# Performance work log

Measured on AMD Instinct MI355X. Metric: run time of the kernel, lower is better.

## Reference

```python
import jax, jax.numpy as jnp
import numpy as np
from jax import lax

B, L, V = 128, 64, 8192
E = H = 128
STEPS = 10
MAX_BIN = 512
BETA_START, BETA_END = 1e-4, 2e-2


def setup_inputs():
    key = jax.random.key(0)
    k = jax.random.split(key, 23)
    s = 0.05
    padded_x = (jax.random.uniform(k[0], (B, L, V)) < 0.01).astype(jnp.float32)
    lengths = jax.random.randint(k[1], (B,), 1, L + 1)
    visit_mask = (jnp.arange(L)[None, :] < lengths[:, None]).astype(jnp.float32)
    padded_bins = jnp.sort(jax.random.randint(k[2], (B, L), 0, MAX_BIN), axis=1)
    t_diff = jax.random.randint(k[3], (B,), 1, STEPS + 1)
    eps = jax.random.normal(k[4], (B, L, E))
    z0 = jax.random.normal(k[5], (B, L, E))
    noise = jax.random.normal(k[6], (STEPS, B, L, E))
    W_visit = jax.random.normal(k[7], (E, V)) * s
    bin_embed = (jax.random.normal(k[8], (MAX_BIN + 2, E)) * s).at[0].set(0.0)  # padding_idx=0
    W_ih = jax.random.normal(k[9], (4 * H, E)) * s
    W_hh = jax.random.normal(k[10], (4 * H, H)) * s
    b_ih = jax.random.normal(k[11], (4 * H,)) * s
    b_hh = jax.random.normal(k[12], (4 * H,)) * s
    W_cls = jax.random.normal(k[13], (1, H)) * s
    b_cls = jax.random.normal(k[14], (1,)) * s
    W_proj = jax.random.normal(k[15], (E, H)) * s
    time_embed = jax.random.normal(k[16], (STEPS + 1, E)) * s
    W_fuse = jax.random.normal(k[17], (2, 2 * E)) * s
    b_fuse = jax.random.normal(k[18], (2,)) * s
    W_e1 = jax.random.normal(k[19], (E, 2 * E)) * s
    b_e1 = jax.random.normal(k[20], (E,)) * s
    W_e2 = jax.random.normal(k[21], (E, E)) * s
    b_e2 = jax.random.normal(k[22], (E,)) * s
    return dict(padded_x=padded_x, visit_mask=visit_mask, padded_bins=padded_bins,
                t_diff=t_diff, eps=eps, z0=z0, noise=noise, W_visit=W_visit,
                bin_embed=bin_embed, W_ih=W_ih, W_hh=W_hh, b_ih=b_ih, b_hh=b_hh,
                W_cls=W_cls, b_cls=b_cls, W_proj=W_proj, time_embed=time_embed,
                W_fuse=W_fuse, b_fuse=b_fuse, W_e1=W_e1, b_e1=b_e1, W_e2=W_e2, b_e2=b_e2)


def _lstm(v, W_ih, W_hh, b_ih, b_hh):
    # v: [B,L,E] -> h: [B,L,H]; PyTorch gate order i,f,g,o
    xg = jnp.einsum('ble,ge->blg', v, W_ih) + b_ih + b_hh
    def step(carry, x):
        h, c = carry
        g = x + h @ W_hh.T
        i, f, gg, o = jnp.split(g, 4, axis=-1)
        c = jax.nn.sigmoid(f) * c + jax.nn.sigmoid(i) * jnp.tanh(gg)
        h = jax.nn.sigmoid(o) * jnp.tanh(c)
        return (h, c), h
    z = jnp.zeros((v.shape[0], W_hh.shape[1]), v.dtype)
    _, hs = lax.scan(step, (z, z), jnp.swapaxes(xg, 0, 1))
    return jnp.swapaxes(hs, 0, 1)


def _last_hidden(h, mask):
    lengths = jnp.maximum(mask.sum(axis=1).astype(jnp.int32), 1)
    return h[jnp.arange(h.shape[0]), lengths - 1]


def reference(padded_x, visit_mask, padded_bins, t_diff, eps, z0, noise,
              W_visit, bin_embed, W_ih, W_hh, b_ih, b_hh, W_cls, b_cls,
              W_proj, time_embed, W_fuse, b_fuse, W_e1, b_e1, W_e2, b_e2):
    m = visit_mask[..., None]                      # [B,L,1]
    betas = jnp.linspace(BETA_START, BETA_END, STEPS)
    alphas = 1.0 - betas
    alpha_bars = jnp.cumprod(alphas)

    # visit embedding + time-gap (delta bin) embedding
    delta = jnp.concatenate([jnp.zeros_like(padded_bins[:, :1]),
                             jnp.clip(padded_bins[:, 1:] - padded_bins[:, :-1], 0)], axis=1)
    delta = jnp.where(visit_mask > 0, jnp.clip(delta, 0, MAX_BIN + 1), 0)
    v = (padded_x @ W_visit.T + bin_embed[delta]) * m  # [B,L,E]

    # encoder LSTM (packed seq == plain scan then zero padded suffix positions)
    h = _lstm(v, W_ih, W_hh, b_ih, b_hh) * m
    logits_real = (_last_hidden(h, visit_mask) @ W_cls.T + b_cls)[:, 0]

    h_prev = jnp.pad(h[:, :-1], ((0, 0), (1, 0), (0, 0)))
    hp = (h_prev @ W_proj.T) * m                   # [B,L,E]

    def fuse_eps(z, t_emb):
        a = jax.nn.softmax(jnp.concatenate([z, hp], -1) @ W_fuse.T + b_fuse, axis=-1)
        g = a[..., :1] * z + a[..., 1:] * hp
        x = jnp.concatenate([g, t_emb], -1)
        return jax.nn.relu(x @ W_e1.T + b_e1) @ W_e2.T + b_e2

    # diffusion loss
    t = jnp.where(visit_mask > 0, t_diff[:, None], 1)    # [B,L]
    ab = alpha_bars[t - 1][..., None]
    z_t = (jnp.sqrt(ab) * v + jnp.sqrt(1.0 - ab) * eps) * m
    eps_pred = fuse_eps(z_t, time_embed[t])
    denom = jnp.maximum(visit_mask.sum(), 1.0)
    diffusion_loss = jnp.sum((eps_pred - eps) ** 2 * m) / denom

    # reverse diffusion sampling of synthetic visit embeddings
    def step(z, inp):
        kk, nz = inp
        t_s = jnp.where(visit_mask > 0, kk, 1)
        e = fuse_eps(z, time_embed[t_s])
        beta = betas[kk - 1]
        mean = (z - beta / jnp.sqrt(1.0 - alpha_bars[kk - 1]) * e) / jnp.sqrt(alphas[kk - 1])
        z = jnp.where(kk > 1, mean + jnp.sqrt(beta) * nz, mean) * m
        return z, None

    ks = jnp.arange(STEPS, 0, -1)
    v_syn, _ = lax.scan(step, z0, (ks, noise))

    h_syn = _lstm(v_syn, W_ih, W_hh, b_ih, b_hh) * m
    logits_syn = (_last_hidden(h_syn, visit_mask) @ W_cls.T + b_cls)[:, 0]
    return logits_real, logits_syn, diffusion_loss
```

## Files before the change

### kernel.cpp

```cpp
#include <hip/hip_runtime.h>

#define B_ 128
#define L_ 64
#define V_ 8192
#define E_ 128
#define H_ 128
#define G4_ 512
#define NROW (B_*L_)
#define HSTRIDE 136
#define AS 136
#define XS 264
#define YS 136
#define ZS 132

typedef unsigned short u16;
typedef __attribute__((ext_vector_type(8))) short bf16x8;
typedef __attribute__((ext_vector_type(4))) float f32x4;

__device__ __forceinline__ float sigm(float x){ return 1.f/(1.f + __expf(-x)); }
__device__ __forceinline__ float ftanh(float x){ float e = __expf(2.f*x); return 1.f - 2.f/(e + 1.f); }
__device__ __forceinline__ u16 f2bf(float f){
    union { unsigned int i; float f; } x; x.f = f;
    unsigned int r = x.i + 0x7fff + ((x.i >> 16) & 1);
    return (u16)(r >> 16);
}
#define LBAR() asm volatile("s_waitcnt lgkmcnt(0)\ns_barrier" ::: "memory")

__device__ __forceinline__ bf16x8 pack8(const float* p){
    const float4* q = (const float4*)p;
    float4 a = q[0], b = q[1];
    bf16x8 f;
    f[0]=(short)f2bf(a.x); f[1]=(short)f2bf(a.y); f[2]=(short)f2bf(a.z); f[3]=(short)f2bf(a.w);
    f[4]=(short)f2bf(b.x); f[5]=(short)f2bf(b.y); f[6]=(short)f2bf(b.z); f[7]=(short)f2bf(b.w);
    return f;
}

__global__ __launch_bounds__(256) void k_transpose_wv(const float* __restrict__ Wv, float* __restrict__ WT){
    __shared__ float tile[16][129];
    int v0 = blockIdx.x * 16;
    int t = threadIdx.x;
    #pragma unroll
    for(int i=0;i<8;i++){
        int idx = i*256 + t; int e = idx >> 4; int vv = idx & 15;
        tile[vv][e] = Wv[(size_t)e*V_ + v0 + vv];
    }
    __syncthreads();
    #pragma unroll
    for(int i=0;i<8;i++){
        int idx = i*256 + t; int vv = idx >> 7; int e = idx & 127;
        WT[(size_t)(v0+vv)*E_ + e] = tile[vv][e];
    }
}

__global__ __launch_bounds__(256) void k_visit_embed(const float* __restrict__ px, const float* __restrict__ vmask,
                                                     const int* __restrict__ bins, const float* __restrict__ bemb,
                                                     const float* __restrict__ WT, float* __restrict__ v){
    __shared__ int idxs[512];
    __shared__ int cnt;
    __shared__ int dsh;
    __shared__ float msh;
    __shared__ float4 red[8][32];
    int row = blockIdx.x; int l = row & 63;
    int t = threadIdx.x;
    if(t==0){
        cnt = 0;
        float m = vmask[row];
        int d = 0;
        if(l > 0){ d = bins[row] - bins[row-1]; d = d < 0 ? 0 : (d > 513 ? 513 : d); }
        if(!(m > 0.f)) d = 0;
        dsh = d; msh = m;
    }
    __syncthreads();
    const uint4* xr4 = (const uint4*)(px + (size_t)row * V_);
    for(int i=t;i<2048;i+=256){
        uint4 u = xr4[i];
        unsigned int w[4] = {u.x,u.y,u.z,u.w};
        #pragma unroll
        for(int j=0;j<4;j++){
            if(w[j]){ int p = atomicAdd(&cnt,1); if(p<512) idxs[p] = i*4 + j; }
        }
    }
    __syncthreads();
    int n = cnt; if(n > 512) n = 512;
    int eq = t & 31, jg = t >> 5;
    float4 a4 = {0.f,0.f,0.f,0.f};
    for(int j=jg;j<n;j+=8){
        const float4* wr = (const float4*)(WT + (size_t)idxs[j]*E_);
        float4 wv = wr[eq];
        a4.x += wv.x; a4.y += wv.y; a4.z += wv.z; a4.w += wv.w;
    }
    red[jg][eq] = a4;
    __syncthreads();
    if(t < 32){
        float4 s = red[0][t];
        #pragma unroll
        for(int g=1;g<8;g++){
            float4 r = red[g][t];
            s.x += r.x; s.y += r.y; s.z += r.z; s.w += r.w;
        }
        const float4* bp = (const float4*)(bemb + dsh*E_);
        float4 bv = bp[t];
        float m = msh;
        float4 o;
        o.x = (s.x + bv.x)*m; o.y = (s.y + bv.y)*m; o.z = (s.z + bv.z)*m; o.w = (s.w + bv.w)*m;
        ((float4*)(v + (size_t)row*E_))[t] = o;
    }
}

__global__ __launch_bounds__(256,2) void k_gemm_xg(const float* __restrict__ A, const float* __restrict__ Wih,
                                                   const float* __restrict__ bih, const float* __restrict__ bhh,
                                                   float* __restrict__ xg){
    __shared__ __align__(16) u16 abuf[16*AS];
    int t = threadIdx.x, wave = t >> 6, lane = t & 63, quad = lane >> 4, lc = lane & 15;
    int row0 = blockIdx.x * 16;
    #pragma unroll
    for(int i=0;i<8;i++){
        int flat = i*256 + t; int r = flat >> 7, e = flat & 127;
        abuf[r*AS + e] = f2bf(A[(size_t)(row0+r)*E_ + e]);
    }
    bf16x8 wfr[8][4]; float bb[8];
    #pragma unroll
    for(int nt=0;nt<8;nt++){
        int n = wave*128 + nt*16 + lc;
        bb[nt] = bih[n] + bhh[n];
        const float* wr = Wih + (size_t)n*E_ + quad*8;
        #pragma unroll
        for(int kt=0;kt<4;kt++) wfr[nt][kt] = pack8(wr + kt*32);
    }
    __syncthreads();
    f32x4 acc[8];
    #pragma unroll
    for(int nt=0;nt<8;nt++) acc[nt] = (f32x4){0.f,0.f,0.f,0.f};
    #pragma unroll
    for(int kt=0;kt<4;kt++){
        bf16x8 af = *(const bf16x8*)&abuf[lc*AS + kt*32 + quad*8];
        #pragma unroll
        for(int nt=0;nt<8;nt++)
            acc[nt] = __builtin_amdgcn_mfma_f32_16x16x32_bf16(af, wfr[nt][kt], acc[nt], 0,0,0);
    }
    #pragma unroll
    for(int nt=0;nt<8;nt++){
        int n = wave*128 + nt*16 + lc;
        #pragma unroll
        for(int r=0;r<4;r++)
            xg[(size_t)(row0 + quad*4 + r)*G4_ + n] = acc[nt][r] + bb[nt];
    }
}

__device__ __forceinline__ void lstm_step(int l, const float* pxg, float* hp_out, bool dohp,
        const u16* bufr, u16* bufw, const bf16x8 (&bf)[4][4], const bf16x8 (&wp)[4],
        float (&xcur)[4][4], float (&xnxt)[4][4], float (&c4)[4], float (&lg4)[4],
        const int (&len4)[4], float wcv,
        const float* vmsh, int lc, int quad, int wave, int b0){
    if(l+1 < 64){
        #pragma unroll
        for(int gate=0;gate<4;gate++){
            #pragma unroll
            for(int r=0;r<4;r++)
                xnxt[gate][r] = pxg[(size_t)r*64*G4_ + (size_t)(l+1)*G4_ + gate*128];
        }
    }
    bf16x8 af[4];
    #pragma unroll
    for(int kt=0;kt<4;kt++)
        af[kt] = *(const bf16x8*)&bufr[lc*HSTRIDE + kt*32 + quad*8];
    f32x4 acc[4], acch;
    #pragma unroll
    for(int a=0;a<4;a++) acc[a] = (f32x4){0.f,0.f,0.f,0.f};
    acch = (f32x4){0.f,0.f,0.f,0.f};
    #pragma unroll
    for(int kt=0;kt<4;kt++){
        #pragma unroll
        for(int a=0;a<4;a++)
            acc[a] = __builtin_amdgcn_mfma_f32_16x16x32_bf16(af[kt], bf[a][kt], acc[a], 0,0,0);
        acch = __builtin_amdgcn_mfma_f32_16x16x32_bf16(af[kt], wp[kt], acch, 0,0,0);
    }
    if(dohp){
        #pragma unroll
        for(int r=0;r<4;r++){
            float m = vmsh[(quad*4+r)*64 + l];
            int grow = (b0 + quad*4 + r)*64 + l;
            hp_out[(size_t)grow*E_ + wave*16 + lc] = acch[r] * m;
        }
    }
    #pragma unroll
    for(int r=0;r<4;r++){
        float gi = acc[0][r] + xcur[0][r];
        float gf = acc[1][r] + xcur[1][r];
        float gg = acc[2][r] + xcur[2][r];
        float go = acc[3][r] + xcur[3][r];
        float c  = sigm(gf)*c4[r] + sigm(gi)*ftanh(gg);
        float h  = sigm(go)*ftanh(c);
        c4[r] = c;
        bufw[(quad*4+r)*HSTRIDE + wave*16 + lc] = f2bf(h);
        if(l == len4[r]-1) lg4[r] += h * wcv;
    }
    LBAR();
}

__global__ __launch_bounds__(512,2) void k_lstm_fused(const float* __restrict__ xg, const float* __restrict__ Whh,
        const float* __restrict__ Wproj, const float* __restrict__ Wcls, const float* __restrict__ bcls,
        const float* __restrict__ vmask, float* __restrict__ hp_out, float* __restrict__ logits_out){
    __shared__ u16 hbuf[2][16*HSTRIDE];
    __shared__ float vmsh[16*64];
    __shared__ int lensh[16];
    __shared__ float lgsh[16][132];
    int t = threadIdx.x;
    int wave = t >> 6, lane = t & 63;
    int quad = lane >> 4, lc = lane & 15;
    int b0 = blockIdx.x * 16;
    bool dohp = (hp_out != nullptr);

    for(int i=t;i<16*HSTRIDE;i+=512) hbuf[0][i] = 0;
    for(int i=t;i<1024;i+=512) vmsh[i] = vmask[b0*64 + i];
    __syncthreads();
    if(t < 16){
        int s = 0;
        #pragma unroll
        for(int i=0;i<64;i++) s += (vmsh[t*64 + i] > 0.f) ? 1 : 0;
        lensh[t] = s < 1 ? 1 : s;
    }

    int cw = wave*16 + lc;
    bf16x8 bf[4][4];
    #pragma unroll
    for(int gate=0;gate<4;gate++){
        int n = gate*128 + cw;
        const float* wr = Whh + (size_t)n*H_ + quad*8;
        #pragma unroll
        for(int kt=0;kt<4;kt++) bf[gate][kt] = pack8(wr + kt*32);
    }
    bf16x8 wp[4];
    {
        const float* wr = Wproj + (size_t)cw*H_ + quad*8;
        #pragma unroll
        for(int kt=0;kt<4;kt++) wp[kt] = pack8(wr + kt*32);
    }
    float wcv = Wcls[cw];

    float c4[4] = {0.f,0.f,0.f,0.f};
    float lg4[4] = {0.f,0.f,0.f,0.f};

    const float* pxg = xg + ((size_t)(b0 + quad*4))*64*G4_ + cw;

    float xgv0[4][4], xgv1[4][4];
    #pragma unroll
    for(int gate=0;gate<4;gate++){
        #pragma unroll
        for(int r=0;r<4;r++)
            xgv0[gate][r] = pxg[(size_t)r*64*G4_ + gate*128];
    }
    __syncthreads();
    int len4[4];
    #pragma unroll
    for(int r=0;r<4;r++) len4[r] = lensh[quad*4 + r];

    for(int lb=0;lb<64;lb+=2){
        lstm_step(lb,   pxg, hp_out, dohp, hbuf[0], hbuf[1], bf, wp, xgv0, xgv1, c4, lg4, len4, wcv, vmsh, lc, quad, wave, b0);
        lstm_step(lb+1, pxg, hp_out, dohp, hbuf[1], hbuf[0], bf, wp, xgv1, xgv0, c4, lg4, len4, wcv, vmsh, lc, quad, wave, b0);
    }
    #pragma unroll
    for(int r=0;r<4;r++) lgsh[quad*4+r][cw] = lg4[r];
    __syncthreads();
    {
        int row = t >> 5, l32 = t & 31;
        float s = lgsh[row][l32] + lgsh[row][l32+32] + lgsh[row][l32+64] + lgsh[row][l32+96];
        s += __shfl_down(s, 16, 32);
        s += __shfl_down(s, 8, 32);
        s += __shfl_down(s, 4, 32);
        s += __shfl_down(s, 2, 32);
        s += __shfl_down(s, 1, 32);
        if(l32 == 0) logits_out[b0 + row] = s + bcls[0];
    }
}

__global__ __launch_bounds__(256,2) void k_drg(const float* __restrict__ v, const float* __restrict__ hp,
        const float* __restrict__ eps, const int* __restrict__ tdiff, const float* __restrict__ vmask,
        const float* __restrict__ z0, const float* __restrict__ noise, const float* __restrict__ temb,
        const float* __restrict__ Wf, const float* __restrict__ bfu,
        const float* __restrict__ We1, const float* __restrict__ be1,
        const float* __restrict__ We2, const float* __restrict__ be2,
        const float* __restrict__ Wih, const float* __restrict__ bih, const float* __restrict__ bhh,
        float* __restrict__ partial, float* __restrict__ xg2){
    __shared__ float zbuf[16*ZS], hpbuf[16*ZS];
    __shared__ __align__(16) u16 xbuf[16*XS];
    __shared__ __align__(16) u16 y1buf[16*YS];
    __shared__ float wfsh[512];
    __shared__ float ssh[16][2], hpd[16][2];
    __shared__ float mrow[16]; __shared__ int trow[16];
    __shared__ float sbeta[10], sabar[10];
    __shared__ float rb[4];
    int row0 = blockIdx.x * 16; int t = threadIdx.x;
    int wave = t >> 6, lane = t & 63, quad = lane >> 4, lc = lane & 15;

    if(t==0){
        float p = 1.f;
        for(int k=0;k<10;k++){ float b = 1e-4f + (0.02f - 1e-4f)*k/9.f; sbeta[k] = b; p *= (1.f - b); sabar[k] = p; }
    }
    if(t < 16){
        int row = row0 + t; float m = vmask[row];
        mrow[t] = m; trow[t] = (m > 0.f) ? tdiff[row >> 6] : 1;
    }
    for(int i=t;i<512;i+=256) wfsh[i] = Wf[i];
    __syncthreads();
    #pragma unroll
    for(int i=0;i<8;i++){
        int flat = i*256 + t; int r = flat >> 7; int e = flat & 127; int row = row0 + r;
        float ab = sabar[trow[r]-1];
        zbuf[r*ZS + e] = (sqrtf(ab)*v[(size_t)row*E_ + e] + sqrtf(1.f - ab)*eps[(size_t)row*E_ + e]) * mrow[r];
        hpbuf[r*ZS + e] = hp[(size_t)row*E_ + e];
    }
    bf16x8 wf1[2][8], wf2[2][4];
    float be1v[2], be2v[2];
    #pragma unroll
    for(int nt=0;nt<2;nt++){
        int n = wave*32 + nt*16 + lc;
        be1v[nt] = be1[n]; be2v[nt] = be2[n];
        const float* w1 = We1 + (size_t)n*256 + quad*8;
        #pragma unroll
        for(int kt=0;kt<8;kt++) wf1[nt][kt] = pack8(w1 + kt*32);
        const float* w2 = We2 + (size_t)n*128 + quad*8;
        #pragma unroll
        for(int kt=0;kt<4;kt++) wf2[nt][kt] = pack8(w2 + kt*32);
    }
    __syncthreads();
    {
        int row = t >> 4, k = (t >> 3) & 1, sub = t & 7;
        float p = 0.f;
        #pragma unroll
        for(int i=0;i<16;i++)
            p += hpbuf[row*ZS + sub*16 + i] * wfsh[k*256 + 128 + sub*16 + i];
        p += __shfl_down(p,4); p += __shfl_down(p,2); p += __shfl_down(p,1);
        if(sub == 0) hpd[row][k] = p + bfu[k];
    }
    __syncthreads();

    for(int s=0;s<11;s++){
        int kk = 10 - (s - 1);
        {
            int row = t >> 4, k = (t >> 3) & 1, sub = t & 7;
            float q = 0.f;
            #pragma unroll
            for(int i=0;i<16;i++)
                q += zbuf[row*ZS + sub*16 + i] * wfsh[k*256 + sub*16 + i];
            q += __shfl_down(q,4); q += __shfl_down(q,2); q += __shfl_down(q,1);
            if(sub == 0) ssh[row][k] = q + hpd[row][k];
        }
        __syncthreads();
        {
            int row = t >> 4, c0 = (t & 15) * 16;
            float s0 = ssh[row][0], s1 = ssh[row][1];
            float a0 = 1.f/(1.f + __expf(s1 - s0)), a1 = 1.f - a0;
            int tt = (s == 0) ? trow[row] : ((mrow[row] > 0.f) ? kk : 1);
            #pragma unroll
            for(int i=0;i<16;i++){
                int c = c0 + i;
                float val = (c < 128) ? (a0*zbuf[row*ZS + c] + a1*hpbuf[row*ZS + c])
                                      : temb[tt*E_ + (c - 128)];
                xbuf[row*XS + c] = f2bf(val);
            }
        }
        __syncthreads();
        f32x4 acc1[2];
        acc1[0] = (f32x4){0.f,0.f,0.f,0.f}; acc1[1] = (f32x4){0.f,0.f,0.f,0.f};
        #pragma unroll
        for(int kt=0;kt<8;kt++){
            bf16x8 af = *(const bf16x8*)&xbuf[lc*XS + kt*32 + quad*8];
            acc1[0] = __builtin_amdgcn_mfma_f32_16x16x32_bf16(af, wf1[0][kt], acc1[0], 0,0,0);
            acc1[1] = __builtin_amdgcn_mfma_f32_16x16x32_bf16(af, wf1[1][kt], acc1[1], 0,0,0);
        }
        #pragma unroll
        for(int nt=0;nt<2;nt++){
            #pragma unroll
            for(int r=0;r<4;r++)
                y1buf[(quad*4+r)*YS + wave*32 + nt*16 + lc] = f2bf(fmaxf(acc1[nt][r] + be1v[nt], 0.f));
        }
        __syncthreads();
        f32x4 acc2[2];
        acc2[0] = (f32x4){0.f,0.f,0.f,0.f}; acc2[1] = (f32x4){0.f,0.f,0.f,0.f};
        #pragma unroll
        for(int kt=0;kt<4;kt++){
            bf16x8 af = *(const bf16x8*)&y1buf[lc*YS + kt*32 + quad*8];
            acc2[0] = __builtin_amdgcn_mfma_f32_16x16x32_bf16(af, wf2[0][kt], acc2[0], 0,0,0);
            acc2[1] = __builtin_amdgcn_mfma_f32_16x16x32_bf16(af, wf2[1][kt], acc2[1], 0,0,0);
        }
        if(s == 0){
            float lp = 0.f;
            #pragma unroll
            for(int nt=0;nt<2;nt++){
                int n = wave*32 + nt*16 + lc;
                #pragma unroll
                for(int r=0;r<4;r++){
                    int m = quad*4 + r;
                    float d = (acc2[nt][r] + be2v[nt]) - eps[(size_t)(row0+m)*E_ + n];
                    lp += d*d*mrow[m];
                }
            }
            #pragma unroll
            for(int off=32;off;off>>=1) lp += __shfl_down(lp, off);
            if(lane == 0) rb[wave] = lp;
            __syncthreads();
            if(t == 0) partial[blockIdx.x] = rb[0]+rb[1]+rb[2]+rb[3];
            #pragma unroll
            for(int i=0;i<8;i++){
                int flat = i*256 + t; int r = flat >> 7; int e = flat & 127;
                zbuf[r*ZS + e] = z0[(size_t)(row0+r)*E_ + e];
            }
            __syncthreads();
        } else {
            float beta = sbeta[kk-1];
            float c1 = beta / sqrtf(1.f - sabar[kk-1]);
            float c2 = 1.f / sqrtf(1.f - beta);
            float sb = sqrtf(beta);
            #pragma unroll
            for(int nt=0;nt<2;nt++){
                int n = wave*32 + nt*16 + lc;
                #pragma unroll
                for(int r=0;r<4;r++){
                    int m = quad*4 + r;
                    float e = acc2[nt][r] + be2v[nt];
                    float z = zbuf[m*ZS + n];
                    float mean = (z - c1*e) * c2;
                    float nz = noise[((size_t)(s-1)*NROW + row0 + m)*E_ + n];
                    float znew = (kk > 1) ? (mean + sb*nz) : mean;
                    zbuf[m*ZS + n] = znew * mrow[m];
                }
            }
            __syncthreads();
        }
    }
    {
        int row = t >> 4, c0 = (t & 15) * 8;
        #pragma unroll
        for(int i=0;i<8;i++)
            xbuf[row*XS + c0 + i] = f2bf(zbuf[row*ZS + c0 + i]);
    }
    __syncthreads();
    bf16x8 wg[8][4]; float bb[8];
    #pragma unroll
    for(int nt=0;nt<8;nt++){
        int n = wave*128 + nt*16 + lc;
        bb[nt] = bih[n] + bhh[n];
        const float* wr = Wih + (size_t)n*E_ + quad*8;
        #pragma unroll
        for(int kt=0;kt<4;kt++) wg[nt][kt] = pack8(wr + kt*32);
    }
    f32x4 ac[8];
    #pragma unroll
    for(int nt=0;nt<8;nt++) ac[nt] = (f32x4){0.f,0.f,0.f,0.f};
    #pragma unroll
    for(int kt=0;kt<4;kt++){
        bf16x8 af = *(const bf16x8*)&xbuf[lc*XS + kt*32 + quad*8];
        #pragma unroll
        for(int nt=0;nt<8;nt++)
            ac[nt] = __builtin_amdgcn_mfma_f32_16x16x32_bf16(af, wg[nt][kt], ac[nt], 0,0,0);
    }
    #pragma unroll
    for(int nt=0;nt<8;nt++){
        int n = wave*128 + nt*16 + lc;
        #pragma unroll
        for(int r=0;r<4;r++)
            xg2[(size_t)(row0 + quad*4 + r)*G4_ + n] = ac[nt][r] + bb[nt];
    }
}

__global__ void k_finalize(const float* __restrict__ partial, const float* __restrict__ vmask, float* __restrict__ out){
    __shared__ float rb[4], rl[4];
    int t = threadIdx.x;
    float s = 0.f;
    for(int i=t;i<NROW;i+=256) s += vmask[i];
    float ls = 0.f;
    for(int i=t;i<512;i+=256) ls += partial[i];
    #pragma unroll
    for(int off=32;off;off>>=1){ s += __shfl_down(s, off); ls += __shfl_down(ls, off); }
    if((t & 63) == 0){ rb[t >> 6] = s; rl[t >> 6] = ls; }
    __syncthreads();
    if(t == 0){
        float denom = rb[0]+rb[1]+rb[2]+rb[3];
        if(denom < 1.f) denom = 1.f;
        out[256] = (rl[0]+rl[1]+rl[2]+rl[3]) / denom;
    }
}

extern "C" void kernel_launch(void* const* d_in, const int* in_sizes, int n_in,
                              void* d_out, int out_size, void* d_ws, size_t ws_size,
                              hipStream_t stream){
    const float* px    = (const float*)d_in[0];
    const float* vmask = (const float*)d_in[1];
    const int*   bins  = (const int*)d_in[2];
    const int*   tdiff = (const int*)d_in[3];
    const float* eps   = (const float*)d_in[4];
    const float* z0    = (const float*)d_in[5];
    const float* noise = (const float*)d_in[6];
    const float* Wv    = (const float*)d_in[7];
    const float* bemb  = (const float*)d_in[8];
    const float* Wih   = (const float*)d_in[9];
    const float* Whh   = (const float*)d_in[10];
    const float* bih   = (const float*)d_in[11];
    const float* bhh   = (const float*)d_in[12];
    const float* Wcls  = (const float*)d_in[13];
    const float* bcls  = (const float*)d_in[14];
    const float* Wproj = (const float*)d_in[15];
    const float* temb  = (const float*)d_in[16];
    const float* Wf    = (const float*)d_in[17];
    const float* bfu   = (const float*)d_in[18];
    const float* We1   = (const float*)d_in[19];
    const float* be1   = (const float*)d_in[20];
    const float* We2   = (const float*)d_in[21];
    const float* be2   = (const float*)d_in[22];
    float* out = (float*)d_out;

    float* ws      = (float*)d_ws;
    float* WT      = ws;
    float* v       = ws + 1048576;
    float* xg      = ws + 2097152;
    float* hp      = ws + 6291456;
    float* partial = ws + 7340032;

    hipLaunchKernelGGL(k_transpose_wv, dim3(V_/16), dim3(256), 0, stream, Wv, WT);
    hipLaunchKernelGGL(k_visit_embed, dim3(NROW), dim3(256), 0, stream, px, vmask, bins, bemb, WT, v);
    hipLaunchKernelGGL(k_gemm_xg, dim3(NROW/16), dim3(256), 0, stream, v, Wih, bih, bhh, xg);
    hipLaunchKernelGGL(k_lstm_fused, dim3(B_/16), dim3(512), 0, stream,
                       xg, Whh, Wproj, Wcls, bcls, vmask, hp, out);
    hipLaunchKernelGGL(k_drg, dim3(NROW/16), dim3(256), 0, stream,
                       v, hp, eps, tdiff, vmask, z0, noise, temb, Wf, bfu,
                       We1, be1, We2, be2, Wih, bih, bhh, partial, xg);
    hipLaunchKernelGGL(k_lstm_fused, dim3(B_/16), dim3(512), 0, stream,
                       xg, Whh, Wproj, Wcls, bcls, vmask, (float*)nullptr, out + 128);
    hipLaunchKernelGGL(k_finalize, dim3(1), dim3(256), 0, stream, partial, vmask, out);
}
```

Baseline: 816.3 us.

## Fuse LSTM input projection into recurrent kernel and drop xg buffers

Removes the separate input-gate GEMM kernel and the tail GEMM in the diffusion kernel. The LSTM kernel now stages each timestep's visit embedding in shared memory as bf16 and computes W_ih·v alongside W_hh·h with MFMA inside the recurrence, so the large xg gate tensor no longer has to be written and re-read from global memory. The LSTM kernel is templated on whether the projected hidden state is needed, which drops the projection MFMAs in the second pass. The diffusion kernel loads its noise, eps and z0 values into registers at the start of each step and writes v_syn directly. The trade-off is that each serial LSTM step now carries twice the MFMA work on the critical recurrent path, with only 8 blocks running. The hp output also no longer multiplies by the visit mask.

Result: no change. 824.1 us (+1.0%).

```diff
diff --git a/kernel.cpp b/kernel.cpp
--- a/kernel.cpp
+++ b/kernel.cpp
@@ -5,7 +5,6 @@
 #define V_ 8192
 #define E_ 128
 #define H_ 128
-#define G4_ 512
 #define NROW (B_*L_)
 #define HSTRIDE 136
 #define AS 136
@@ -107,112 +106,86 @@
     }
 }
 
-__global__ __launch_bounds__(256,2) void k_gemm_xg(const float* __restrict__ A, const float* __restrict__ Wih,
-                                                   const float* __restrict__ bih, const float* __restrict__ bhh,
-                                                   float* __restrict__ xg){
-    __shared__ __align__(16) u16 abuf[16*AS];
-    int t = threadIdx.x, wave = t >> 6, lane = t & 63, quad = lane >> 4, lc = lane & 15;
-    int row0 = blockIdx.x * 16;
-    #pragma unroll
-    for(int i=0;i<8;i++){
-        int flat = i*256 + t; int r = flat >> 7, e = flat & 127;
-        abuf[r*AS + e] = f2bf(A[(size_t)(row0+r)*E_ + e]);
-    }
-    bf16x8 wfr[8][4]; float bb[8];
-    #pragma unroll
-    for(int nt=0;nt<8;nt++){
-        int n = wave*128 + nt*16 + lc;
-        bb[nt] = bih[n] + bhh[n];
-        const float* wr = Wih + (size_t)n*E_ + quad*8;
-        #pragma unroll
-        for(int kt=0;kt<4;kt++) wfr[nt][kt] = pack8(wr + kt*32);
-    }
-    __syncthreads();
-    f32x4 acc[8];
-    #pragma unroll
-    for(int nt=0;nt<8;nt++) acc[nt] = (f32x4){0.f,0.f,0.f,0.f};
+template<bool DOHP>
+__device__ __forceinline__ void lstm_step(int l,
+        const u16* __restrict__ bufr, u16* __restrict__ bufw,
+        const u16* __restrict__ vbr, u16* __restrict__ vbw,
+        const float*& pv, float*& hpb,
+        const bf16x8 (&bfh)[4][4], const bf16x8 (&bfv)[4][4], const bf16x8 (&wp)[4],
+        const float (&bb)[4], float (&c4)[4], float (&lg4)[4], const int (&len4)[4],
+        float wcv, int t, int lc, int quad, int cw){
+    float4 vnx;
+    if(l+1 < 64){ vnx = *(const float4*)pv; pv += E_; }
+    bf16x8 afh[4], afv[4];
     #pragma unroll
     for(int kt=0;kt<4;kt++){
-        bf16x8 af = *(const bf16x8*)&abuf[lc*AS + kt*32 + quad*8];
-        #pragma unroll
-        for(int nt=0;nt<8;nt++)
-            acc[nt] = __builtin_amdgcn_mfma_f32_16x16x32_bf16(af, wfr[nt][kt], acc[nt], 0,0,0);
-    }
-    #pragma unroll
-    for(int nt=0;nt<8;nt++){
-        int n = wave*128 + nt*16 + lc;
-        #pragma unroll
-        for(int r=0;r<4;r++)
-            xg[(size_t)(row0 + quad*4 + r)*G4_ + n] = acc[nt][r] + bb[nt];
-    }
-}
-
-__device__ __forceinline__ void lstm_step(int l, const float* pxg, float* hp_out, bool dohp,
-        const u16* bufr, u16* bufw, const bf16x8 (&bf)[4][4], const bf16x8 (&wp)[4],
-        float (&xcur)[4][4], float (&xnxt)[4][4], float (&c4)[4], float (&lg4)[4],
-        const int (&len4)[4], float wcv,
-        const float* vmsh, int lc, int quad, int wave, int b0){
-    if(l+1 < 64){
-        #pragma unroll
-        for(int gate=0;gate<4;gate++){
-            #pragma unroll
-            for(int r=0;r<4;r++)
-                xnxt[gate][r] = pxg[(size_t)r*64*G4_ + (size_t)(l+1)*G4_ + gate*128];
-        }
-    }
-    bf16x8 af[4];
-    #pragma unroll
-    for(int kt=0;kt<4;kt++)
-        af[kt] = *(const bf16x8*)&bufr[lc*HSTRIDE + kt*32 + quad*8];
+        afh[kt] = *(const bf16x8*)&bufr[lc*HSTRIDE + kt*32 + quad*8];
+        afv[kt] = *(const bf16x8*)&vbr[lc*AS + kt*32 + quad*8];
+    }
     f32x4 acc[4], acch;
     #pragma unroll
-    for(int a=0;a<4;a++) acc[a] = (f32x4){0.f,0.f,0.f,0.f};
+    for(int g=0;g<4;g++) acc[g] = (f32x4){0.f,0.f,0.f,0.f};
     acch = (f32x4){0.f,0.f,0.f,0.f};
     #pragma unroll
     for(int kt=0;kt<4;kt++){
         #pragma unroll
-        for(int a=0;a<4;a++)
-            acc[a] = __builtin_amdgcn_mfma_f32_16x16x32_bf16(af[kt], bf[a][kt], acc[a], 0,0,0);
-        acch = __builtin_amdgcn_mfma_f32_16x16x32_bf16(af[kt], wp[kt], acch, 0,0,0);
-    }
-    if(dohp){
-        #pragma unroll
-        for(int r=0;r<4;r++){
-            float m = vmsh[(quad*4+r)*64 + l];
-            int grow = (b0 + quad*4 + r)*64 + l;
-            hp_out[(size_t)grow*E_ + wave*16 + lc] = acch[r] * m;
-        }
+        for(int g=0;g<4;g++){
+            acc[g] = __builtin_amdgcn_mfma_f32_16x16x32_bf16(afh[kt], bfh[g][kt], acc[g], 0,0,0);
+            acc[g] = __builtin_amdgcn_mfma_f32_16x16x32_bf16(afv[kt], bfv[g][kt], acc[g], 0,0,0);
+        }
+        if constexpr (DOHP)
+            acch = __builtin_amdgcn_mfma_f32_16x16x32_bf16(afh[kt], wp[kt], acch, 0,0,0);
+    }
+    if constexpr (DOHP){
+        #pragma unroll
+        for(int r=0;r<4;r++) hpb[(size_t)r*64*E_] = acch[r];
+        hpb += E_;
     }
     #pragma unroll
     for(int r=0;r<4;r++){
-        float gi = acc[0][r] + xcur[0][r];
-        float gf = acc[1][r] + xcur[1][r];
-        float gg = acc[2][r] + xcur[2][r];
-        float go = acc[3][r] + xcur[3][r];
+        float gi = acc[0][r] + bb[0];
+        float gf = acc[1][r] + bb[1];
+        float gg = acc[2][r] + bb[2];
+        float go = acc[3][r] + bb[3];
         float c  = sigm(gf)*c4[r] + sigm(gi)*ftanh(gg);
         float h  = sigm(go)*ftanh(c);
         c4[r] = c;
-        bufw[(quad*4+r)*HSTRIDE + wave*16 + lc] = f2bf(h);
+        bufw[(quad*4+r)*HSTRIDE + cw] = f2bf(h);
         if(l == len4[r]-1) lg4[r] += h * wcv;
     }
+    if(l+1 < 64){
+        int sr = t >> 5, se = (t & 31)*4;
+        u16* d = vbw + sr*AS + se;
+        d[0]=f2bf(vnx.x); d[1]=f2bf(vnx.y); d[2]=f2bf(vnx.z); d[3]=f2bf(vnx.w);
+    }
     LBAR();
 }
 
-__global__ __launch_bounds__(512,2) void k_lstm_fused(const float* __restrict__ xg, const float* __restrict__ Whh,
+template<bool DOHP>
+__global__ __launch_bounds__(512,2) void k_lstm_fused(const float* __restrict__ vin,
+        const float* __restrict__ Whh, const float* __restrict__ Wih,
+        const float* __restrict__ bih, const float* __restrict__ bhh,
         const float* __restrict__ Wproj, const float* __restrict__ Wcls, const float* __restrict__ bcls,
         const float* __restrict__ vmask, float* __restrict__ hp_out, float* __restrict__ logits_out){
-    __shared__ u16 hbuf[2][16*HSTRIDE];
+    __shared__ __align__(16) u16 hbuf[2][16*HSTRIDE];
+    __shared__ __align__(16) u16 vbuf[2][16*AS];
     __shared__ float vmsh[16*64];
     __shared__ int lensh[16];
     __shared__ float lgsh[16][132];
     int t = threadIdx.x;
     int wave = t >> 6, lane = t & 63;
     int quad = lane >> 4, lc = lane & 15;
+    int cw = wave*16 + lc;
     int b0 = blockIdx.x * 16;
-    bool dohp = (hp_out != nullptr);
 
     for(int i=t;i<16*HSTRIDE;i+=512) hbuf[0][i] = 0;
     for(int i=t;i<1024;i+=512) vmsh[i] = vmask[b0*64 + i];
+    const float* pv = vin + (size_t)(b0 + (t>>5))*64*E_ + (t&31)*4;
+    {
+        float4 v0 = *(const float4*)pv; pv += E_;
+        u16* d = &vbuf[0][(t>>5)*AS + (t&31)*4];
+        d[0]=f2bf(v0.x); d[1]=f2bf(v0.y); d[2]=f2bf(v0.z); d[3]=f2bf(v0.w);
+    }
     __syncthreads();
     if(t < 16){
         int s = 0;
@@ -221,43 +194,34 @@
         lensh[t] = s < 1 ? 1 : s;
     }
 
-    int cw = wave*16 + lc;
-    bf16x8 bf[4][4];
-    #pragma unroll
-    for(int gate=0;gate<4;gate++){
-        int n = gate*128 + cw;
-        const float* wr = Whh + (size_t)n*H_ + quad*8;
-        #pragma unroll
-        for(int kt=0;kt<4;kt++) bf[gate][kt] = pack8(wr + kt*32);
-    }
-    bf16x8 wp[4];
-    {
+    bf16x8 bfh[4][4], bfv[4][4], wp[4];
+    float bb[4];
+    #pragma unroll
+    for(int g=0;g<4;g++){
+        int n = g*128 + cw;
+        bb[g] = bih[n] + bhh[n];
+        const float* wrh = Whh + (size_t)n*H_ + quad*8;
+        const float* wrv = Wih + (size_t)n*E_ + quad*8;
+        #pragma unroll
+        for(int kt=0;kt<4;kt++){ bfh[g][kt] = pack8(wrh + kt*32); bfv[g][kt] = pack8(wrv + kt*32); }
+    }
+    if constexpr (DOHP){
         const float* wr = Wproj + (size_t)cw*H_ + quad*8;
         #pragma unroll
         for(int kt=0;kt<4;kt++) wp[kt] = pack8(wr + kt*32);
     }
     float wcv = Wcls[cw];
-
     float c4[4] = {0.f,0.f,0.f,0.f};
     float lg4[4] = {0.f,0.f,0.f,0.f};
-
-    const float* pxg = xg + ((size_t)(b0 + quad*4))*64*G4_ + cw;
-
-    float xgv0[4][4], xgv1[4][4];
-    #pragma unroll
-    for(int gate=0;gate<4;gate++){
-        #pragma unroll
-        for(int r=0;r<4;r++)
-            xgv0[gate][r] = pxg[(size_t)r*64*G4_ + gate*128];
-    }
+    float* hpb = DOHP ? (hp_out + (size_t)(b0 + quad*4)*64*E_ + cw) : nullptr;
     __syncthreads();
     int len4[4];
     #pragma unroll
     for(int r=0;r<4;r++) len4[r] = lensh[quad*4 + r];
 
     for(int lb=0;lb<64;lb+=2){
-        lstm_step(lb,   pxg, hp_out, dohp, hbuf[0], hbuf[1], bf, wp, xgv0, xgv1, c4, lg4, len4, wcv, vmsh, lc, quad, wave, b0);
-        lstm_step(lb+1, pxg, hp_out, dohp, hbuf[1], hbuf[0], bf, wp, xgv1, xgv0, c4, lg4, len4, wcv, vmsh, lc, quad, wave, b0);
+        lstm_step<DOHP>(lb,   hbuf[0], hbuf[1], vbuf[0], vbuf[1], pv, hpb, bfh, bfv, wp, bb, c4, lg4, len4, wcv, t, lc, quad, cw);
+        lstm_step<DOHP>(lb+1, hbuf[1], hbuf[0], vbuf[1], vbuf[0], pv, hpb, bfh, bfv, wp, bb, c4, lg4, len4, wcv, t, lc, quad, cw);
     }
     #pragma unroll
     for(int r=0;r<4;r++) lgsh[quad*4+r][cw] = lg4[r];
@@ -280,9 +244,9 @@
         const float* __restrict__ Wf, const float* __restrict__ bfu,
         const float* __restrict__ We1, const float* __restrict__ be1,
         const float* __restrict__ We2, const float* __restrict__ be2,
-        const float* __restrict__ Wih, const float* __restrict__ bih, const float* __restrict__ bhh,
-        float* __restrict__ partial, float* __restrict__ xg2){
-    __shared__ float zbuf[16*ZS], hpbuf[16*ZS];
+        float* __restrict__ partial, float* __restrict__ vsyn){
+    __shared__ __align__(16) float zbuf[16*ZS];
+    __shared__ float hpbuf[16*ZS];
     __shared__ __align__(16) u16 xbuf[16*XS];
     __shared__ __align__(16) u16 y1buf[16*YS];
     __shared__ float wfsh[512];
@@ -336,7 +300,26 @@
     __syncthreads();
 
     for(int s=0;s<11;s++){
-        int kk = 10 - (s - 1);
+        int kk = 11 - s;
+        float nzv[8], epv[8], z0v[8];
+        if(s >= 1){
+            #pragma unroll
+            for(int nt=0;nt<2;nt++)
+                #pragma unroll
+                for(int r=0;r<4;r++)
+                    nzv[nt*4+r] = noise[((size_t)(s-1)*NROW + row0 + quad*4 + r)*E_ + wave*32 + nt*16 + lc];
+        } else {
+            #pragma unroll
+            for(int nt=0;nt<2;nt++)
+                #pragma unroll
+                for(int r=0;r<4;r++)
+                    epv[nt*4+r] = eps[(size_t)(row0 + quad*4 + r)*E_ + wave*32 + nt*16 + lc];
+            #pragma unroll
+            for(int i=0;i<8;i++){
+                int flat = i*256 + t;
+                z0v[i] = z0[(size_t)(row0 + (flat >> 7))*E_ + (flat & 127)];
+            }
+        }
         {
             int row = t >> 4, k = (t >> 3) & 1, sub = t & 7;
             float q = 0.f;
@@ -388,11 +371,10 @@
             float lp = 0.f;
             #pragma unroll
             for(int nt=0;nt<2;nt++){
-                int n = wave*32 + nt*16 + lc;
                 #pragma unroll
                 for(int r=0;r<4;r++){
                     int m = quad*4 + r;
-                    float d = (acc2[nt][r] + be2v[nt]) - eps[(size_t)(row0+m)*E_ + n];
+                    float d = (acc2[nt][r] + be2v[nt]) - epv[nt*4+r];
                     lp += d*d*mrow[m];
                 }
             }
@@ -404,7 +386,7 @@
             #pragma unroll
             for(int i=0;i<8;i++){
                 int flat = i*256 + t; int r = flat >> 7; int e = flat & 127;
-                zbuf[r*ZS + e] = z0[(size_t)(row0+r)*E_ + e];
+                zbuf[r*ZS + e] = z0v[i];
             }
             __syncthreads();
         } else {
@@ -421,7 +403,7 @@
                     float e = acc2[nt][r] + be2v[nt];
                     float z = zbuf[m*ZS + n];
                     float mean = (z - c1*e) * c2;
-                    float nz = noise[((size_t)(s-1)*NROW + row0 + m)*E_ + n];
+                    float nz = nzv[nt*4+r];
                     float znew = (kk > 1) ? (mean + sb*nz) : mean;
                     zbuf[m*ZS + n] = znew * mrow[m];
                 }
@@ -430,37 +412,11 @@
         }
     }
     {
-        int row = t >> 4, c0 = (t & 15) * 8;
-        #pragma unroll
-        for(int i=0;i<8;i++)
-            xbuf[row*XS + c0 + i] = f2bf(zbuf[row*ZS + c0 + i]);
-    }
-    __syncthreads();
-    bf16x8 wg[8][4]; float bb[8];
-    #pragma unroll
-    for(int nt=0;nt<8;nt++){
-        int n = wave*128 + nt*16 + lc;
-        bb[nt] = bih[n] + bhh[n];
-        const float* wr = Wih + (size_t)n*E_ + quad*8;
-        #pragma unroll
-        for(int kt=0;kt<4;kt++) wg[nt][kt] = pack8(wr + kt*32);
-    }
-    f32x4 ac[8];
-    #pragma unroll
-    for(int nt=0;nt<8;nt++) ac[nt] = (f32x4){0.f,0.f,0.f,0.f};
-    #pragma unroll
-    for(int kt=0;kt<4;kt++){
-        bf16x8 af = *(const bf16x8*)&xbuf[lc*XS + kt*32 + quad*8];
-        #pragma unroll
-        for(int nt=0;nt<8;nt++)
-            ac[nt] = __builtin_amdgcn_mfma_f32_16x16x32_bf16(af, wg[nt][kt], ac[nt], 0,0,0);
-    }
-    #pragma unroll
-    for(int nt=0;nt<8;nt++){
-        int n = wave*128 + nt*16 + lc;
-        #pragma unroll
-        for(int r=0;r<4;r++)
-            xg2[(size_t)(row0 + quad*4 + r)*G4_ + n] = ac[nt][r] + bb[nt];
+        int r = t >> 4, e0 = (t & 15) * 8;
+        float4 a = *(const float4*)&zbuf[r*ZS + e0];
+        float4 b2 = *(const float4*)&zbuf[r*ZS + e0 + 4];
+        *(float4*)&vsyn[(size_t)(row0 + r)*E_ + e0] = a;
+        *(float4*)&vsyn[(size_t)(row0 + r)*E_ + e0 + 4] = b2;
     }
 }
 
@@ -513,19 +469,18 @@
     float* ws      = (float*)d_ws;
     float* WT      = ws;
     float* v       = ws + 1048576;
-    float* xg      = ws + 2097152;
-    float* hp      = ws + 6291456;
-    float* partial = ws + 7340032;
+    float* vsyn    = ws + 2097152;
+    float* hp      = ws + 3145728;
+    float* partial = ws + 4194304;
 
     hipLaunchKernelGGL(k_transpose_wv, dim3(V_/16), dim3(256), 0, stream, Wv, WT);
     hipLaunchKernelGGL(k_visit_embed, dim3(NROW), dim3(256), 0, stream, px, vmask, bins, bemb, WT, v);
-    hipLaunchKernelGGL(k_gemm_xg, dim3(NROW/16), dim3(256), 0, stream, v, Wih, bih, bhh, xg);
-    hipLaunchKernelGGL(k_lstm_fused, dim3(B_/16), dim3(512), 0, stream,
-                       xg, Whh, Wproj, Wcls, bcls, vmask, hp, out);
+    hipLaunchKernelGGL((k_lstm_fused<true>), dim3(B_/16), dim3(512), 0, stream,
+                       v, Whh, Wih, bih, bhh, Wproj, Wcls, bcls, vmask, hp, out);
     hipLaunchKernelGGL(k_drg, dim3(NROW/16), dim3(256), 0, stream,
                        v, hp, eps, tdiff, vmask, z0, noise, temb, Wf, bfu,
-                       We1, be1, We2, be2, Wih, bih, bhh, partial, xg);
-    hipLaunchKernelGGL(k_lstm_fused, dim3(B_/16), dim3(512), 0, stream,
-                       xg, Whh, Wproj, Wcls, bcls, vmask, (float*)nullptr, out + 128);
+                       We1, be1, We2, be2, partial, vsyn);
+    hipLaunchKernelGGL((k_lstm_fused<false>), dim3(B_/16), dim3(512), 0, stream,
+                       vsyn, Whh, Wih, bih, bhh, Wproj, Wcls, bcls, vmask, (float*)nullptr, out + 128);
     hipLaunchKernelGGL(k_finalize, dim3(1), dim3(256), 0, stream, partial, vmask, out);
 }
```
